# Kernel optimization log

Measured on AMD Instinct MI355X. Metric: run time of the kernel, lower is better.

Reference implementation:

```python
import jax, jax.numpy as jnp
import numpy as np

TEMPERATURE = 0.9  # DiversityLoss temperature
EPS = 1e-6


def setup_inputs() -> dict:
    key = jax.random.key(0)
    kx, ke = jax.random.split(key)
    x = jax.random.normal(kx, (8, 4096, 128), dtype=jnp.float32)
    embed = jax.random.normal(ke, (2048, 128), dtype=jnp.float32)  # [codebook_size, dim]
    return {"x": x, "embed": embed}


def reference(x, embed):
    """EuclideanCodebook.forward (ema_update=True, eval mode: no buffer updates).

    Returns (quantize, embed_ind, diversity_loss).
    """
    shape = x.shape
    xf = x.reshape(-1, shape[-1])                       # [N, d]
    x_sq = jnp.sum(xf * xf, axis=1, keepdims=True)      # [N, 1]
    e_sq = jnp.sum(embed * embed, axis=1)[None, :]      # [1, K]
    confidence = -(x_sq - 2.0 * (xf @ embed.T) + e_sq)  # [N, K]
    embed_ind_flat = jnp.argmax(confidence, axis=-1)    # [N]
    # dequantize: gather codebook rows, restore leading shape
    quantize = jnp.take(embed, embed_ind_flat, axis=0).reshape(shape)
    embed_ind = embed_ind_flat.reshape(shape[:-1])
    # diversity loss: softmax over codes per point, mean over points, entropy-style sum
    point_probs = jax.nn.softmax(confidence / TEMPERATURE, axis=1)  # [N, K]
    class_probs = jnp.mean(point_probs, axis=0)                      # [K]
    diversity_loss = jnp.sum(class_probs * jnp.log(class_probs + EPS))
    return quantize, embed_ind, diversity_loss
```

## Files before the change

### kernel.cpp

```cpp
#include <hip/hip_runtime.h>
#include <math.h>

#define D        128
#define KCODES   2048
#define NPTS     32768
#define LO_SCALE 4096.0f
#define C1       3.205988979753252f
#define C2       (C1 / LO_SCALE)
#define ESQ_SCALE 1.602994489876626f

#define A_CSLICES 4
#define A_CODES   512
#define A_NCH     (A_CODES / 32)

#define SW(G, r)  (((G) ^ (r)) & 15)

typedef _Float16 half8 __attribute__((ext_vector_type(8)));
typedef float    f32x4 __attribute__((ext_vector_type(4)));

__device__ __forceinline__ void split_row_part(const float* __restrict__ src,
                                               _Float16* __restrict__ hi_row,
                                               _Float16* __restrict__ lo_row,
                                               int part, int rkey, float* ss) {
    #pragma unroll
    for (int g = 0; g < 4; ++g) {
        const int G = part * 4 + g;
        half8 h, l;
        float s = 0.0f;
        #pragma unroll
        for (int j = 0; j < 8; ++j) {
            float v = src[g * 8 + j];
            _Float16 hh = (_Float16)v;
            h[j] = hh;
            l[j] = (_Float16)((v - (float)hh) * LO_SCALE);
            s += v * v;
        }
        *ss += s;
        const int slot = SW(G, rkey);
        *(half8*)(hi_row + slot * 8) = h;
        *(half8*)(lo_row + slot * 8) = l;
    }
}

__global__ void prep_kernel(const float* __restrict__ embed, const float* __restrict__ x,
                            float* __restrict__ e_sqt,
                            _Float16* __restrict__ ehi, _Float16* __restrict__ elo,
                            _Float16* __restrict__ xhi, _Float16* __restrict__ xlo,
                            float* __restrict__ cacc) {
    const int b = blockIdx.x;
    const int tid = threadIdx.x;
    const int part = tid & 3;
    float ss = 0.0f;
    if (b < KCODES / 64) {
        const int row = b * 64 + (tid >> 2);
        split_row_part(embed + (size_t)row * D + part * 32,
                       ehi + (size_t)row * D, elo + (size_t)row * D, part, row & 15, &ss);
        ss += __shfl_xor(ss, 1, 64);
        ss += __shfl_xor(ss, 2, 64);
        if (part == 0) e_sqt[row] = ss * ESQ_SCALE;
        if (part == 1) cacc[row] = 0.0f;
    } else {
        const int row = (b - KCODES / 64) * 64 + (tid >> 2);
        split_row_part(x + (size_t)row * D + part * 32,
                       xhi + (size_t)row * D, xlo + (size_t)row * D, part, row & 15, &ss);
    }
}

__device__ __forceinline__ void dma32(const _Float16* __restrict__ g_base,
                                      _Float16* lds_base, int row0, int w, int lane) {
    const char* src = (const char*)g_base + (size_t)(row0 + 8 * w) * 256 + lane * 16;
    char* dst = (char*)lds_base + 8 * w * 256;
    #pragma unroll
    for (int i = 0; i < 2; ++i) {
        __builtin_amdgcn_global_load_lds(
            (const __attribute__((address_space(1))) unsigned int*)(src + i * 1024),
            (__attribute__((address_space(3))) unsigned int*)(dst + i * 1024),
            16, 0, 0);
    }
}

__device__ __forceinline__ void load_a(const _Float16* __restrict__ xhi_g,
                                       const _Float16* __restrict__ xlo_g,
                                       int p0w, int col, int quad,
                                       half8 ahi[2][4], half8 alo[2][4]) {
    #pragma unroll
    for (int pt = 0; pt < 2; ++pt) {
        const int pr = p0w + pt * 16 + col;
        #pragma unroll
        for (int kk = 0; kk < 4; ++kk) {
            const int slot = SW(kk * 4 + quad, col);
            ahi[pt][kk] = *(const half8*)(xhi_g + (size_t)pr * D + slot * 8);
            alo[pt][kk] = *(const half8*)(xlo_g + (size_t)pr * D + slot * 8);
        }
    }
}

__global__ __launch_bounds__(256, 2)
void sweepA_kernel(const _Float16* __restrict__ xhi_g, const _Float16* __restrict__ xlo_g,
                   const _Float16* __restrict__ ehi_g, const _Float16* __restrict__ elo_g,
                   const float* __restrict__ e_sqt_g,
                   float* __restrict__ pm, float* __restrict__ pl, int* __restrict__ pidx) {
    __shared__ _Float16 EHI[2][32 * D];
    __shared__ _Float16 ELO[2][32 * D];
    __shared__ float esq_s[A_CODES];

    const int tid  = threadIdx.x;
    const int w    = tid >> 6;
    const int lane = tid & 63;
    const int col  = lane & 15;
    const int quad = lane >> 4;
    const int c0   = blockIdx.y * A_CODES;
    const int p0w  = blockIdx.x * 128 + w * 32;

    dma32(ehi_g, EHI[0], c0, w, lane);
    dma32(elo_g, ELO[0], c0, w, lane);
    for (int i = tid; i < A_CODES; i += 256) esq_s[i] = e_sqt_g[c0 + i];

    half8 ahi[2][4], alo[2][4];
    load_a(xhi_g, xlo_g, p0w, col, quad, ahi, alo);

    float lrun[2][4], bv[2][4];
    int   bi[2][4];
    #pragma unroll
    for (int pt = 0; pt < 2; ++pt)
        #pragma unroll
        for (int r = 0; r < 4; ++r) { lrun[pt][r] = 0.f; bv[pt][r] = -INFINITY; bi[pt][r] = 0; }

    __syncthreads();

    for (int ch = 0; ch < A_NCH; ++ch) {
        const int cur = ch & 1;
        if (ch + 1 < A_NCH) {
            dma32(ehi_g, EHI[cur ^ 1], c0 + (ch + 1) * 32, w, lane);
            dma32(elo_g, ELO[cur ^ 1], c0 + (ch + 1) * 32, w, lane);
        }
        const _Float16* eh = EHI[cur];
        const _Float16* el = ELO[cur];

        #pragma unroll
        for (int ct = 0; ct < 2; ++ct) {
            f32x4 chh[2], cx[2];
            #pragma unroll
            for (int pt = 0; pt < 2; ++pt) { chh[pt] = (f32x4){0,0,0,0}; cx[pt] = (f32x4){0,0,0,0}; }
            #pragma unroll
            for (int kk = 0; kk < 4; ++kk) {
                const int boff = (ct * 16 + col) * D + SW(kk * 4 + quad, col) * 8;
                half8 Bhi = *(const half8*)&eh[boff];
                half8 Blo = *(const half8*)&el[boff];
                #pragma unroll
                for (int pt = 0; pt < 2; ++pt) {
                    chh[pt] = __builtin_amdgcn_mfma_f32_16x16x32_f16(ahi[pt][kk], Bhi, chh[pt], 0, 0, 0);
                    cx[pt]  = __builtin_amdgcn_mfma_f32_16x16x32_f16(ahi[pt][kk], Blo, cx[pt], 0, 0, 0);
                    cx[pt]  = __builtin_amdgcn_mfma_f32_16x16x32_f16(alo[pt][kk], Bhi, cx[pt], 0, 0, 0);
                }
            }
            const int lcode = ch * 32 + ct * 16 + col;
            const float esqT = esq_s[lcode];
            const int gcode = c0 + lcode;
            #pragma unroll
            for (int pt = 0; pt < 2; ++pt) {
                #pragma unroll
                for (int r = 0; r < 4; ++r) {
                    float s2 = fmaf(chh[pt][r], C1, fmaf(cx[pt][r], C2, -esqT));
                    lrun[pt][r] += exp2f(s2);
                    if (s2 > bv[pt][r]) { bv[pt][r] = s2; bi[pt][r] = gcode; }
                }
            }
        }
        __syncthreads();
    }

    #pragma unroll
    for (int pt = 0; pt < 2; ++pt) {
        #pragma unroll
        for (int r = 0; r < 4; ++r) {
            float v = bv[pt][r]; int idx = bi[pt][r]; float l = lrun[pt][r];
            #pragma unroll
            for (int off = 8; off >= 1; off >>= 1) {
                float ov = __shfl_xor(v, off, 16);
                int   oi = __shfl_xor(idx, off, 16);
                float ol = __shfl_xor(l, off, 16);
                l += ol;
                if (ov > v || (ov == v && oi < idx)) { v = ov; idx = oi; }
            }
            if (col == 0) {
                size_t o = (size_t)blockIdx.y * NPTS + p0w + pt * 16 + quad * 4 + r;
                pm[o] = v; pl[o] = l; pidx[o] = idx;
            }
        }
    }
}

__global__ void combine_kernel(const float* __restrict__ pm, const float* __restrict__ pl,
                               const int* __restrict__ pidx,
                               float* __restrict__ r_buf, int* __restrict__ idx_buf,
                               float* __restrict__ ind_out) {
    const int p = blockIdx.x * 256 + threadIdx.x;
    float bm = -INFINITY; int bi = 0; float l = 0.0f;
    #pragma unroll
    for (int sl = 0; sl < A_CSLICES; ++sl) {
        size_t o = (size_t)sl * NPTS + p;
        float v = pm[o];
        l += pl[o];
        if (v > bm) { bm = v; bi = pidx[o]; }
    }
    r_buf[p] = 1.0f / l;
    idx_buf[p] = bi;
    ind_out[p] = (float)bi;
}

__global__ __launch_bounds__(256, 2)
void sweepB_kernel(const _Float16* __restrict__ xhi_g, const _Float16* __restrict__ xlo_g,
                   const _Float16* __restrict__ ehi_g, const _Float16* __restrict__ elo_g,
                   const float* __restrict__ e_sqt_g, const float* __restrict__ r_buf,
                   float* __restrict__ classacc) {
    __shared__ _Float16 EHI[2][32 * D];
    __shared__ _Float16 ELO[2][32 * D];
    __shared__ float esq_s[A_CODES];
    __shared__ float bins[A_CODES];

    const int tid  = threadIdx.x;
    const int w    = tid >> 6;
    const int lane = tid & 63;
    const int col  = lane & 15;
    const int quad = lane >> 4;
    const int c0   = blockIdx.y * A_CODES;
    const int p0w  = blockIdx.x * 128 + w * 32;

    dma32(ehi_g, EHI[0], c0, w, lane);
    dma32(elo_g, ELO[0], c0, w, lane);
    for (int i = tid; i < A_CODES; i += 256) { esq_s[i] = e_sqt_g[c0 + i]; bins[i] = 0.0f; }

    half8 ahi[2][4], alo[2][4];
    load_a(xhi_g, xlo_g, p0w, col, quad, ahi, alo);

    float rr[2][4];
    #pragma unroll
    for (int pt = 0; pt < 2; ++pt)
        #pragma unroll
        for (int r = 0; r < 4; ++r)
            rr[pt][r] = r_buf[p0w + pt * 16 + quad * 4 + r];

    __syncthreads();

    for (int ch = 0; ch < A_NCH; ++ch) {
        const int cur = ch & 1;
        if (ch + 1 < A_NCH) {
            dma32(ehi_g, EHI[cur ^ 1], c0 + (ch + 1) * 32, w, lane);
            dma32(elo_g, ELO[cur ^ 1], c0 + (ch + 1) * 32, w, lane);
        }
        const _Float16* eh = EHI[cur];
        const _Float16* el = ELO[cur];

        #pragma unroll
        for (int ct = 0; ct < 2; ++ct) {
            f32x4 chh[2], cx[2];
            #pragma unroll
            for (int pt = 0; pt < 2; ++pt) { chh[pt] = (f32x4){0,0,0,0}; cx[pt] = (f32x4){0,0,0,0}; }
            #pragma unroll
            for (int kk = 0; kk < 4; ++kk) {
                const int boff = (ct * 16 + col) * D + SW(kk * 4 + quad, col) * 8;
                half8 Bhi = *(const half8*)&eh[boff];
                half8 Blo = *(const half8*)&el[boff];
                #pragma unroll
                for (int pt = 0; pt < 2; ++pt) {
                    chh[pt] = __builtin_amdgcn_mfma_f32_16x16x32_f16(ahi[pt][kk], Bhi, chh[pt], 0, 0, 0);
                    cx[pt]  = __builtin_amdgcn_mfma_f32_16x16x32_f16(ahi[pt][kk], Blo, cx[pt], 0, 0, 0);
                    cx[pt]  = __builtin_amdgcn_mfma_f32_16x16x32_f16(alo[pt][kk], Bhi, cx[pt], 0, 0, 0);
                }
            }
            const int lcode = ch * 32 + ct * 16 + col;
            const float esqT = esq_s[lcode];
            float wsum = 0.0f;
            #pragma unroll
            for (int pt = 0; pt < 2; ++pt) {
                #pragma unroll
                for (int r = 0; r < 4; ++r) {
                    float s2 = fmaf(chh[pt][r], C1, fmaf(cx[pt][r], C2, -esqT));
                    wsum += exp2f(s2) * rr[pt][r];
                }
            }
            wsum += __shfl_xor(wsum, 16, 64);
            wsum += __shfl_xor(wsum, 32, 64);
            if (quad == 0) atomicAdd(&bins[lcode], wsum);
        }
        __syncthreads();
    }

    for (int i = tid; i < A_CODES; i += 256)
        atomicAdd(&classacc[c0 + i], bins[i]);
}

__global__ void gather_kernel(const float* __restrict__ embed,
                              const int* __restrict__ idx_buf,
                              float* __restrict__ q_out) {
    const int j = blockIdx.x * 256 + threadIdx.x;
    const int row = j >> 5;
    const int d4 = j & 31;
    reinterpret_cast<float4*>(q_out)[(size_t)row * 32 + d4] =
        reinterpret_cast<const float4*>(embed)[(size_t)idx_buf[row] * 32 + d4];
}

__global__ void finalize_kernel(const float* __restrict__ classacc,
                                float* __restrict__ loss_out, int N, int K) {
    __shared__ float red[256];
    const int tid = threadIdx.x;
    float s = 0.0f;
    const float invN = 1.0f / (float)N;
    for (int i = tid; i < K; i += 256) {
        float cp = classacc[i] * invN;
        s += cp * logf(cp + 1e-6f);
    }
    red[tid] = s;
    __syncthreads();
    for (int off = 128; off > 0; off >>= 1) {
        if (tid < off) red[tid] += red[tid + off];
        __syncthreads();
    }
    if (tid == 0) loss_out[0] = red[0];
}

extern "C" void kernel_launch(void* const* d_in, const int* in_sizes, int n_in,
                              void* d_out, int out_size, void* d_ws, size_t ws_size,
                              hipStream_t stream) {
    const float* x     = (const float*)d_in[0];
    const float* embed = (const float*)d_in[1];

    float* out      = (float*)d_out;
    float* q_out    = out;
    float* ind_out  = out + (size_t)NPTS * D;
    float* loss_out = ind_out + NPTS;

    float*    e_sqt = (float*)d_ws;
    float*    cacc  = e_sqt + KCODES;
    _Float16* ehi   = (_Float16*)(cacc + KCODES);
    _Float16* elo   = ehi + (size_t)KCODES * D;
    _Float16* xhi   = elo + (size_t)KCODES * D;
    _Float16* xlo   = xhi + (size_t)NPTS * D;
    float*    pm    = (float*)(xlo + (size_t)NPTS * D);
    float*    pl    = pm + (size_t)A_CSLICES * NPTS;
    int*      pidx  = (int*)(pl + (size_t)A_CSLICES * NPTS);
    float*    r_buf = (float*)(pidx + (size_t)A_CSLICES * NPTS);
    int*      idx_buf = (int*)(r_buf + NPTS);

    prep_kernel<<<KCODES / 64 + NPTS / 64, 256, 0, stream>>>(
        embed, x, e_sqt, ehi, elo, xhi, xlo, cacc);
    sweepA_kernel<<<dim3(NPTS / 128, A_CSLICES), 256, 0, stream>>>(
        xhi, xlo, ehi, elo, e_sqt, pm, pl, pidx);
    combine_kernel<<<NPTS / 256, 256, 0, stream>>>(pm, pl, pidx, r_buf, idx_buf, ind_out);
    sweepB_kernel<<<dim3(NPTS / 128, A_CSLICES), 256, 0, stream>>>(
        xhi, xlo, ehi, elo, e_sqt, r_buf, cacc);
    gather_kernel<<<NPTS * 32 / 256, 256, 0, stream>>>(embed, idx_buf, q_out);
    finalize_kernel<<<1, 256, 0, stream>>>(cacc, loss_out, NPTS, KCODES);
}
```

Measured before the change: 207.5 us.

## Fuse combine and gather into sweepB, halve code slices, double LDS chunk

Removes the separate combine and gather kernels. sweepB now merges the per-slice max, sum and index itself into shared memory and writes the quantized rows and indices from the y==0 slice. It also halves the code slices from 4 to 2 of 1024 codes each and doubles the embed chunk staged in LDS to 64 codes, which halves the grid and doubles the LDS footprint per block. The intent is to save kernel launches and global round trips, at the cost of less parallelism and possibly fewer resident blocks per CU.

```diff
diff --git a/kernel.cpp b/kernel.cpp
--- a/kernel.cpp
+++ b/kernel.cpp
@@ -9,9 +9,10 @@
 #define C2       (C1 / LO_SCALE)
 #define ESQ_SCALE 1.602994489876626f
 
-#define A_CSLICES 4
-#define A_CODES   512
-#define A_NCH     (A_CODES / 32)
+#define A_CSLICES 2
+#define A_CODES   1024
+#define CHUNK     64
+#define A_NCH     (A_CODES / CHUNK)
 
 #define SW(G, r)  (((G) ^ (r)) & 15)
 
@@ -66,12 +67,12 @@
     }
 }
 
-__device__ __forceinline__ void dma32(const _Float16* __restrict__ g_base,
+__device__ __forceinline__ void dma64(const _Float16* __restrict__ g_base,
                                       _Float16* lds_base, int row0, int w, int lane) {
-    const char* src = (const char*)g_base + (size_t)(row0 + 8 * w) * 256 + lane * 16;
-    char* dst = (char*)lds_base + 8 * w * 256;
-    #pragma unroll
-    for (int i = 0; i < 2; ++i) {
+    const char* src = (const char*)g_base + (size_t)(row0 + 16 * w) * 256 + lane * 16;
+    char* dst = (char*)lds_base + 16 * w * 256;
+    #pragma unroll
+    for (int i = 0; i < 4; ++i) {
         __builtin_amdgcn_global_load_lds(
             (const __attribute__((address_space(1))) unsigned int*)(src + i * 1024),
             (__attribute__((address_space(3))) unsigned int*)(dst + i * 1024),
@@ -100,8 +101,8 @@
                    const _Float16* __restrict__ ehi_g, const _Float16* __restrict__ elo_g,
                    const float* __restrict__ e_sqt_g,
                    float* __restrict__ pm, float* __restrict__ pl, int* __restrict__ pidx) {
-    __shared__ _Float16 EHI[2][32 * D];
-    __shared__ _Float16 ELO[2][32 * D];
+    __shared__ _Float16 EHI[2][CHUNK * D];
+    __shared__ _Float16 ELO[2][CHUNK * D];
     __shared__ float esq_s[A_CODES];
 
     const int tid  = threadIdx.x;
@@ -112,8 +113,8 @@
     const int c0   = blockIdx.y * A_CODES;
     const int p0w  = blockIdx.x * 128 + w * 32;
 
-    dma32(ehi_g, EHI[0], c0, w, lane);
-    dma32(elo_g, ELO[0], c0, w, lane);
+    dma64(ehi_g, EHI[0], c0, w, lane);
+    dma64(elo_g, ELO[0], c0, w, lane);
     for (int i = tid; i < A_CODES; i += 256) esq_s[i] = e_sqt_g[c0 + i];
 
     half8 ahi[2][4], alo[2][4];
@@ -131,14 +132,14 @@
     for (int ch = 0; ch < A_NCH; ++ch) {
         const int cur = ch & 1;
         if (ch + 1 < A_NCH) {
-            dma32(ehi_g, EHI[cur ^ 1], c0 + (ch + 1) * 32, w, lane);
-            dma32(elo_g, ELO[cur ^ 1], c0 + (ch + 1) * 32, w, lane);
+            dma64(ehi_g, EHI[cur ^ 1], c0 + (ch + 1) * CHUNK, w, lane);
+            dma64(elo_g, ELO[cur ^ 1], c0 + (ch + 1) * CHUNK, w, lane);
         }
         const _Float16* eh = EHI[cur];
         const _Float16* el = ELO[cur];
 
         #pragma unroll
-        for (int ct = 0; ct < 2; ++ct) {
+        for (int ct = 0; ct < 4; ++ct) {
             f32x4 chh[2], cx[2];
             #pragma unroll
             for (int pt = 0; pt < 2; ++pt) { chh[pt] = (f32x4){0,0,0,0}; cx[pt] = (f32x4){0,0,0,0}; }
@@ -154,7 +155,7 @@
                     cx[pt]  = __builtin_amdgcn_mfma_f32_16x16x32_f16(alo[pt][kk], Bhi, cx[pt], 0, 0, 0);
                 }
             }
-            const int lcode = ch * 32 + ct * 16 + col;
+            const int lcode = ch * CHUNK + ct * 16 + col;
             const float esqT = esq_s[lcode];
             const int gcode = c0 + lcode;
             #pragma unroll
@@ -191,33 +192,20 @@
     }
 }
 
-__global__ void combine_kernel(const float* __restrict__ pm, const float* __restrict__ pl,
-                               const int* __restrict__ pidx,
-                               float* __restrict__ r_buf, int* __restrict__ idx_buf,
-                               float* __restrict__ ind_out) {
-    const int p = blockIdx.x * 256 + threadIdx.x;
-    float bm = -INFINITY; int bi = 0; float l = 0.0f;
-    #pragma unroll
-    for (int sl = 0; sl < A_CSLICES; ++sl) {
-        size_t o = (size_t)sl * NPTS + p;
-        float v = pm[o];
-        l += pl[o];
-        if (v > bm) { bm = v; bi = pidx[o]; }
-    }
-    r_buf[p] = 1.0f / l;
-    idx_buf[p] = bi;
-    ind_out[p] = (float)bi;
-}
-
 __global__ __launch_bounds__(256, 2)
 void sweepB_kernel(const _Float16* __restrict__ xhi_g, const _Float16* __restrict__ xlo_g,
                    const _Float16* __restrict__ ehi_g, const _Float16* __restrict__ elo_g,
-                   const float* __restrict__ e_sqt_g, const float* __restrict__ r_buf,
-                   float* __restrict__ classacc) {
-    __shared__ _Float16 EHI[2][32 * D];
-    __shared__ _Float16 ELO[2][32 * D];
+                   const float* __restrict__ e_sqt_g,
+                   const float* __restrict__ pm, const float* __restrict__ pl,
+                   const int* __restrict__ pidx,
+                   float* __restrict__ classacc, const float* __restrict__ embed,
+                   float* __restrict__ q_out, float* __restrict__ ind_out) {
+    __shared__ _Float16 EHI[2][CHUNK * D];
+    __shared__ _Float16 ELO[2][CHUNK * D];
     __shared__ float esq_s[A_CODES];
     __shared__ float bins[A_CODES];
+    __shared__ float r_s[128];
+    __shared__ int   idx_s[128];
 
     const int tid  = threadIdx.x;
     const int w    = tid >> 6;
@@ -225,35 +213,51 @@
     const int col  = lane & 15;
     const int quad = lane >> 4;
     const int c0   = blockIdx.y * A_CODES;
-    const int p0w  = blockIdx.x * 128 + w * 32;
-
-    dma32(ehi_g, EHI[0], c0, w, lane);
-    dma32(elo_g, ELO[0], c0, w, lane);
+    const int p0   = blockIdx.x * 128;
+    const int p0w  = p0 + w * 32;
+
+    dma64(ehi_g, EHI[0], c0, w, lane);
+    dma64(elo_g, ELO[0], c0, w, lane);
     for (int i = tid; i < A_CODES; i += 256) { esq_s[i] = e_sqt_g[c0 + i]; bins[i] = 0.0f; }
+
+    if (tid < 128) {
+        const int p = p0 + tid;
+        float bm = -INFINITY; int bidx = 0; float l = 0.0f;
+        #pragma unroll
+        for (int sl = 0; sl < A_CSLICES; ++sl) {
+            size_t o = (size_t)sl * NPTS + p;
+            float v = pm[o];
+            l += pl[o];
+            if (v > bm) { bm = v; bidx = pidx[o]; }
+        }
+        r_s[tid] = 1.0f / l;
+        idx_s[tid] = bidx;
+        if (blockIdx.y == 0) ind_out[p] = (float)bidx;
+    }
 
     half8 ahi[2][4], alo[2][4];
     load_a(xhi_g, xlo_g, p0w, col, quad, ahi, alo);
 
+    __syncthreads();
+
     float rr[2][4];
     #pragma unroll
     for (int pt = 0; pt < 2; ++pt)
         #pragma unroll
         for (int r = 0; r < 4; ++r)
-            rr[pt][r] = r_buf[p0w + pt * 16 + quad * 4 + r];
-
-    __syncthreads();
+            rr[pt][r] = r_s[w * 32 + pt * 16 + quad * 4 + r];
 
     for (int ch = 0; ch < A_NCH; ++ch) {
         const int cur = ch & 1;
         if (ch + 1 < A_NCH) {
-            dma32(ehi_g, EHI[cur ^ 1], c0 + (ch + 1) * 32, w, lane);
-            dma32(elo_g, ELO[cur ^ 1], c0 + (ch + 1) * 32, w, lane);
+            dma64(ehi_g, EHI[cur ^ 1], c0 + (ch + 1) * CHUNK, w, lane);
+            dma64(elo_g, ELO[cur ^ 1], c0 + (ch + 1) * CHUNK, w, lane);
         }
         const _Float16* eh = EHI[cur];
         const _Float16* el = ELO[cur];
 
         #pragma unroll
-        for (int ct = 0; ct < 2; ++ct) {
+        for (int ct = 0; ct < 4; ++ct) {
             f32x4 chh[2], cx[2];
             #pragma unroll
             for (int pt = 0; pt < 2; ++pt) { chh[pt] = (f32x4){0,0,0,0}; cx[pt] = (f32x4){0,0,0,0}; }
@@ -269,7 +273,7 @@
                     cx[pt]  = __builtin_amdgcn_mfma_f32_16x16x32_f16(alo[pt][kk], Bhi, cx[pt], 0, 0, 0);
                 }
             }
-            const int lcode = ch * 32 + ct * 16 + col;
+            const int lcode = ch * CHUNK + ct * 16 + col;
             const float esqT = esq_s[lcode];
             float wsum = 0.0f;
             #pragma unroll
@@ -289,16 +293,17 @@
 
     for (int i = tid; i < A_CODES; i += 256)
         atomicAdd(&classacc[c0 + i], bins[i]);
-}
-
-__global__ void gather_kernel(const float* __restrict__ embed,
-                              const int* __restrict__ idx_buf,
-                              float* __restrict__ q_out) {
-    const int j = blockIdx.x * 256 + threadIdx.x;
-    const int row = j >> 5;
-    const int d4 = j & 31;
-    reinterpret_cast<float4*>(q_out)[(size_t)row * 32 + d4] =
-        reinterpret_cast<const float4*>(embed)[(size_t)idx_buf[row] * 32 + d4];
+
+    if (blockIdx.y == 0) {
+        const float4* emb4 = (const float4*)embed;
+        float4* q4 = (float4*)q_out;
+        #pragma unroll
+        for (int it = 0; it < 16; ++it) {
+            int j = tid + it * 256;
+            int row = j >> 5, d4 = j & 31;
+            q4[(size_t)(p0 + row) * 32 + d4] = emb4[(size_t)idx_s[row] * 32 + d4];
+        }
+    }
 }
 
 __global__ void finalize_kernel(const float* __restrict__ classacc,
@@ -340,16 +345,12 @@
     float*    pm    = (float*)(xlo + (size_t)NPTS * D);
     float*    pl    = pm + (size_t)A_CSLICES * NPTS;
     int*      pidx  = (int*)(pl + (size_t)A_CSLICES * NPTS);
-    float*    r_buf = (float*)(pidx + (size_t)A_CSLICES * NPTS);
-    int*      idx_buf = (int*)(r_buf + NPTS);
 
     prep_kernel<<<KCODES / 64 + NPTS / 64, 256, 0, stream>>>(
         embed, x, e_sqt, ehi, elo, xhi, xlo, cacc);
     sweepA_kernel<<<dim3(NPTS / 128, A_CSLICES), 256, 0, stream>>>(
         xhi, xlo, ehi, elo, e_sqt, pm, pl, pidx);
-    combine_kernel<<<NPTS / 256, 256, 0, stream>>>(pm, pl, pidx, r_buf, idx_buf, ind_out);
     sweepB_kernel<<<dim3(NPTS / 128, A_CSLICES), 256, 0, stream>>>(
-        xhi, xlo, ehi, elo, e_sqt, r_buf, cacc);
-    gather_kernel<<<NPTS * 32 / 256, 256, 0, stream>>>(embed, idx_buf, q_out);
+        xhi, xlo, ehi, elo, e_sqt, pm, pl, pidx, cacc, embed, q_out, ind_out);
     finalize_kernel<<<1, 256, 0, stream>>>(cacc, loss_out, NPTS, KCODES);
 }
```

After: 203.8 us. Within noise of the previous version (-1.8%).
